# Kernel optimization log

Hardware: AMD Instinct MI355X
Metric: run time of the kernel (lower is better)

## Reference

```python
import jax, jax.numpy as jnp
import numpy as np

B, T, H, L, AS = 64, 256, 1024, 3, 128  # batch, seq-1, hidden, layers, alphabet


def setup_inputs() -> dict:
    key = jax.random.key(0)
    ks = jax.random.split(key, 8)
    # one-hot character sequence (B, T, AS), float32
    idx = jax.random.randint(ks[0], (B, T), 0, AS)
    sequence = jax.nn.one_hot(idx, AS, dtype=jnp.float32)
    u = lambda k, shape, fan: jax.random.uniform(
        k, shape, minval=-1.0 / np.sqrt(fan), maxval=1.0 / np.sqrt(fan), dtype=jnp.float32)
    W_i2h = u(ks[1], (H, AS), AS)
    b_i2h = u(ks[2], (H,), AS)
    # per-layer LSTM params, PyTorch gate order [i, f, g, o]; layer inputs all have width H
    W_ih = u(ks[3], (L, 4 * H, H), H)
    W_hh = u(ks[4], (L, 4 * H, H), H)
    b_ih = u(ks[5], (L, 4 * H), H)
    b_hh = u(ks[6], (L, 4 * H), H)
    W_h2O = u(ks[7], (AS, H), H)
    b_h2O = jnp.zeros((AS,), dtype=jnp.float32)
    h0 = jnp.zeros((L, B, H), dtype=jnp.float32)
    c0 = jnp.zeros((L, B, H), dtype=jnp.float32)
    return dict(sequence=sequence, W_i2h=W_i2h, b_i2h=b_i2h, W_ih=W_ih, W_hh=W_hh,
                b_ih=b_ih, b_hh=b_hh, W_h2O=W_h2O, b_h2O=b_h2O, h0=h0, c0=c0)


def _lstm_layer(x, h0, c0, W_ih, W_hh, b_ih, b_hh):
    # x: (B, T, H). Precompute input contribution to the gates for all steps.
    xg = jnp.einsum('bth,gh->btg', x, W_ih) + b_ih  # (B, T, 4H)

    def step(carry, xg_t):
        h, c = carry
        gates = xg_t + h @ W_hh.T + b_hh  # (B, 4H)
        i, f, g, o = jnp.split(gates, 4, axis=-1)
        c = jax.nn.sigmoid(f) * c + jax.nn.sigmoid(i) * jnp.tanh(g)
        h = jax.nn.sigmoid(o) * jnp.tanh(c)
        return (h, c), h

    (hT, cT), hs = jax.lax.scan(step, (h0, c0), jnp.swapaxes(xg, 0, 1))
    return jnp.swapaxes(hs, 0, 1), hT, cT  # (B,T,H), (B,H), (B,H)


def reference(sequence, W_i2h, b_i2h, W_ih, W_hh, b_ih, b_hh, W_h2O, b_h2O, h0, c0):
    # i2h projection
    x = jnp.einsum('bta,ha->bth', sequence, W_i2h) + b_i2h  # (B, T, H)
    # multi-layer LSTM over x (eval mode: the dropout=True arg is inactive in eval)
    inp = x
    h_fin, c_fin = [], []
    for l in range(L):
        inp, hT, cT = _lstm_layer(inp, h0[l], c0[l], W_ih[l], W_hh[l], b_ih[l], b_hh[l])
        h_fin.append(hT)
        c_fin.append(cT)
    # NOTE: faithful to the original code's bug -- h2O is applied to the i2h
    # output `x`, not to the LSTM output. The LSTM only produces the new hidden.
    out = x.reshape(-1, H) @ W_h2O.T + b_h2O  # (B*T, AS)
    return out, jnp.stack(h_fin), jnp.stack(c_fin)
```

## Files before the change

kernel.cpp:

```cpp
#include <hip/hip_runtime.h>
#include <stdint.h>
#include <stddef.h>

#define B_  64
#define T_  256
#define H_  1024
#define AS_ 128
#define L_  3

typedef __attribute__((ext_vector_type(8))) short bf16x8;
typedef __attribute__((ext_vector_type(4))) float f32x4;
typedef __attribute__((ext_vector_type(4))) unsigned u32x4;

__device__ __forceinline__ unsigned short f2bf(float f) {
  union { float f; unsigned u; } x; x.f = f;
  unsigned r = x.u + 0x7fffu + ((x.u >> 16) & 1u);
  return (unsigned short)(r >> 16);
}
__device__ __forceinline__ float bf2f(unsigned short s) {
  union { unsigned u; float f; } x; x.u = ((unsigned)s) << 16; return x.f;
}
__device__ __forceinline__ float sigmf(float x) { return 1.0f / (1.0f + __expf(-x)); }
__device__ __forceinline__ float tanh_f(float x) {
  x = fminf(fmaxf(x, -15.0f), 15.0f);
  float e = __expf(2.0f * x);
  return (e - 1.0f) / (e + 1.0f);
}

__device__ __forceinline__ void st_u16_cc(unsigned short* p, unsigned short v) {
  __hip_atomic_store(p, v, __ATOMIC_RELAXED, __HIP_MEMORY_SCOPE_AGENT);
}
__device__ __forceinline__ void st_u32_cc(unsigned* p, unsigned v) {
  __hip_atomic_store(p, v, __ATOMIC_RELAXED, __HIP_MEMORY_SCOPE_AGENT);
}
__device__ __forceinline__ unsigned ld_u32_cc(const unsigned* p) {
  return __hip_atomic_load(p, __ATOMIC_RELAXED, __HIP_MEMORY_SCOPE_AGENT);
}
__device__ __forceinline__ u32x4 ld_b128_cc_nw(const void* p) {
  u32x4 r;
  asm volatile("global_load_dwordx4 %0, %1, off sc0 sc1" : "=v"(r) : "v"(p));
  return r;
}
__device__ __forceinline__ void st_b128_cc_nw(void* p, u32x4 v) {
  asm volatile("global_store_dwordx4 %0, %1, off sc0 sc1" :: "v"(p), "v"(v) : "memory");
}
__device__ __forceinline__ void wait_vm4_tie4(u32x4& a, u32x4& b, u32x4& c, u32x4& d) {
  asm volatile("s_waitcnt vmcnt(4)"
               : "+v"(a), "+v"(b), "+v"(c), "+v"(d) :: "memory");
  __builtin_amdgcn_sched_barrier(0);
}
__device__ __forceinline__ void wait_vm0_tie4(u32x4& a, u32x4& b, u32x4& c, u32x4& d) {
  asm volatile("s_waitcnt vmcnt(0)"
               : "+v"(a), "+v"(b), "+v"(c), "+v"(d) :: "memory");
  __builtin_amdgcn_sched_barrier(0);
}
__device__ __forceinline__ void lds_barrier() {
  __builtin_amdgcn_sched_barrier(0);
  asm volatile("s_waitcnt lgkmcnt(0)" ::: "memory");
  __builtin_amdgcn_sched_barrier(0);
  __builtin_amdgcn_s_barrier();
  __builtin_amdgcn_sched_barrier(0);
}


__global__ void k_prep(unsigned* __restrict__ zp, int nzero,
                       const float* __restrict__ Wi2h, const float* __restrict__ bi2h,
                       unsigned short* __restrict__ Wt,
                       const float* __restrict__ Wih, unsigned short* __restrict__ Wihb, int nwih,
                       const float* __restrict__ Wh2o, unsigned short* __restrict__ Wh2ob,
                       const float* __restrict__ bih, const float* __restrict__ bhh,
                       float* __restrict__ bsum) {
  int i = blockIdx.x * 256 + threadIdx.x;
  if (i < nzero) { st_u32_cc(zp + i, 0u); return; }
  i -= nzero;
  if (i < AS_ * H_) { int a = i >> 10, h = i & 1023; Wt[i] = f2bf(Wi2h[h * AS_ + a] + bi2h[h]); return; }
  i -= AS_ * H_;
  if (i < nwih) { Wihb[i] = f2bf(Wih[i]); return; }
  i -= nwih;
  if (i < AS_ * H_) { Wh2ob[i] = f2bf(Wh2o[i]); return; }
  i -= AS_ * H_;
  if (i < L_ * 4 * H_) bsum[i] = bih[i] + bhh[i];
}

__global__ __launch_bounds__(128) void k_gather(const float* __restrict__ seq,
                                                const unsigned short* __restrict__ Wt,
                                                unsigned short* __restrict__ xbf) {
  __shared__ int sidx;
  const int bt = blockIdx.x, tid = threadIdx.x;
  if (seq[(size_t)bt * AS_ + tid] > 0.5f) sidx = tid;
  __syncthreads();
  const int b = bt >> 8, t = bt & 255;
  const uint4* s = (const uint4*)(Wt + (size_t)sidx * H_);
  uint4* d = (uint4*)(xbf + ((size_t)t * B_ + b) * H_);
  d[tid] = s[tid];
}


__device__ __forceinline__ void gld16(const void* g, void* l) {
  __builtin_amdgcn_global_load_lds((const __attribute__((address_space(1))) unsigned int*)g,
                                   (__attribute__((address_space(3))) unsigned int*)l,
                                   16, 0, 0);
}

template <int OUT>
__device__ __forceinline__ void gemm_tile(const unsigned short* __restrict__ A,
                                          const unsigned short* __restrict__ Bm,
                                          const float* __restrict__ bias,
                                          void* __restrict__ Cout,
                                          int m0, int n0, int K, int N, int tid,
                                          unsigned short* As, unsigned short* Bs) {
  const int lane = tid & 63, wv = tid >> 6;
  const int wr = wv >> 1, wc = wv & 1;
  const int kg = lane >> 4, li = lane & 15;
  f32x4 acc[4][4] = {};

  for (int k0 = 0; k0 < K; k0 += 32) {
    for (int i = 0; i < 2; ++i) {
      int c0 = i * 256 + wv * 64;
      int cid = c0 + lane;
      int row = cid >> 2, lc = cid & 3;
      int sc = lc ^ ((row >> 1) & 3);
      gld16(A + (size_t)(m0 + row) * K + k0 + sc * 8, (char*)As + (size_t)c0 * 16);
      gld16(Bm + (size_t)(n0 + row) * K + k0 + sc * 8, (char*)Bs + (size_t)c0 * 16);
    }
    __syncthreads();
    bf16x8 af[4], bfm[4];
#pragma unroll
    for (int mi = 0; mi < 4; ++mi) {
      int row = wr * 64 + mi * 16 + li;
      int pc = kg ^ ((row >> 1) & 3);
      af[mi] = *(const bf16x8*)((const char*)As + row * 64 + pc * 16);
    }
#pragma unroll
    for (int ni = 0; ni < 4; ++ni) {
      int row = wc * 64 + ni * 16 + li;
      int pc = kg ^ ((row >> 1) & 3);
      bfm[ni] = *(const bf16x8*)((const char*)Bs + row * 64 + pc * 16);
    }
#pragma unroll
    for (int mi = 0; mi < 4; ++mi)
#pragma unroll
      for (int ni = 0; ni < 4; ++ni)
        acc[mi][ni] = __builtin_amdgcn_mfma_f32_16x16x32_bf16(af[mi], bfm[ni], acc[mi][ni], 0, 0, 0);
    __syncthreads();
  }

#pragma unroll
  for (int mi = 0; mi < 4; ++mi)
#pragma unroll
    for (int ni = 0; ni < 4; ++ni)
#pragma unroll
      for (int r = 0; r < 4; ++r) {
        int row = m0 + wr * 64 + mi * 16 + kg * 4 + r;
        int col = n0 + wc * 64 + ni * 16 + li;
        float v = acc[mi][ni][r] + bias[col];
        int tt = row >> 6, b = row & 63;
        if (OUT == 4) {
          ((float*)Cout)[(size_t)(b * 256 + tt) * N + col] = v;
        } else {
          int g = col >> 10, u = col & 1023;
          int idx = ((tt * 4 + (b >> 4)) << 16) | ((u >> 5) << 11) |
                    ((b & 15) << 7) | ((u & 31) << 2) | g;
          ((unsigned short*)Cout)[idx] = f2bf(v);
        }
      }
}

template <int OUT>
__global__ __launch_bounds__(256) void k_gemm(const unsigned short* __restrict__ A,
                                              const unsigned short* __restrict__ Bm,
                                              const float* __restrict__ bias,
                                              void* __restrict__ Cout,
                                              int M, int N, int K) {
  __shared__ __align__(16) unsigned short As[128 * 32];
  __shared__ __align__(16) unsigned short Bs[128 * 32];
  gemm_tile<OUT>(A, Bm, bias, Cout, blockIdx.x * 128, blockIdx.y * 128,
                 K, N, threadIdx.x, As, Bs);
}


__global__ __launch_bounds__(256, 1) void k_fused(
    const unsigned short* __restrict__ xgs,
    const float* __restrict__ Whh,
    unsigned short* __restrict__ h_pp,
    unsigned short* __restrict__ out_seq,
    float* __restrict__ hT, float* __restrict__ cT,
    const float* __restrict__ h0, const float* __restrict__ c0,
    unsigned* __restrict__ slots,
    const unsigned short* __restrict__ WihbN,
    const float* __restrict__ bsumN,
    unsigned short* __restrict__ xgs_out,
    const unsigned short* __restrict__ outA,
    const unsigned short* __restrict__ WoutB,
    const float* __restrict__ bout,
    float* __restrict__ outC) {
  __shared__ __align__(16) unsigned short Wlds[64 * 1024];
  __shared__ __align__(16) unsigned short Hs[16 * 1024];
  const int tid = threadIdx.x, lane = tid & 63, w = tid >> 6;
  const int wg = blockIdx.x;

  if (wg >= 128) {
    const int Wp = wg - 128;
    unsigned short* As = Wlds;
    unsigned short* Bs = Wlds + 4096;
    if (outA)
      gemm_tile<4>(outA, WoutB, bout, (void*)outC, Wp * 128, 0, H_, AS_, tid, As, Bs);
    if (WihbN) {
      const int pline = (Wp & 31) * 32;
      for (int k = 0; k < 32; ++k) {
        const int gidx = Wp + k * 128;
        const int mt = gidx >> 5, nt = gidx & 31;
        const unsigned tgt = (unsigned)(2 * mt + 3);
        if (w == 0) {
          const unsigned* base = slots + (lane >> 4) * 1024 + pline + (lane & 15);
          unsigned v0, v1;
          do {
            __builtin_amdgcn_s_sleep(4);
            v0 = ld_u32_cc(base);
            v1 = ld_u32_cc(base + 16);
          } while (__any((int)((v0 < tgt) | (v1 < tgt))));
        }
        __syncthreads();
        gemm_tile<2>(out_seq, WihbN, bsumN, (void*)xgs_out,
                     mt * 128, nt * 128, H_, 4 * H_, tid, As, Bs);
      }
    }
    return;
  }

  const int gb = wg >> 5, ug = wg & 31;
  const int li = lane & 15, kq = lane >> 4;
  const int b  = gb * 16 + li;
  const int u0 = ug * 32 + w * 8 + kq;
  const int u1 = u0 + 4;

  st_u16_cc(&h_pp[((size_t)B_ + b) * H_ + u0], f2bf(h0[(size_t)b * H_ + u0]));
  st_u16_cc(&h_pp[((size_t)B_ + b) * H_ + u1], f2bf(h0[(size_t)b * H_ + u1]));

  bf16x8 afr[32];
  {
    const int r0 = w * 32 + li;
    const float* wr = Whh + ((size_t)(r0 & 3) * H_ + ug * 32 + (r0 >> 2)) * H_ + kq * 8;
#pragma unroll
    for (int ks = 0; ks < 32; ++ks) {
      const float4 f0 = *(const float4*)(wr + ks * 32);
      const float4 f1 = *(const float4*)(wr + ks * 32 + 4);
      union { ushort4 a[2]; bf16x8 v; } uu_;
      uu_.a[0] = ushort4{f2bf(f0.x), f2bf(f0.y), f2bf(f0.z), f2bf(f0.w)};
      uu_.a[1] = ushort4{f2bf(f1.x), f2bf(f1.y), f2bf(f1.z), f2bf(f1.w)};
      afr[ks] = uu_.v;
    }
  }
  for (int it = 0; it < 16; ++it) {
    const int r = w * 32 + 16 + it;
    const float* wr = Whh + ((size_t)(r & 3) * H_ + ug * 32 + (r >> 2)) * H_;
#pragma unroll
    for (int j = 0; j < 4; ++j) {
      const float4 f = *(const float4*)(wr + lane * 16 + j * 4);
      ushort4 p = ushort4{f2bf(f.x), f2bf(f.y), f2bf(f.z), f2bf(f.w)};
      const int k = lane * 16 + j * 4;
      *(ushort4*)((char*)Wlds + (size_t)(w * 16 + it) * 2048 + ((2 * k) ^ ((it & 7) << 4))) = p;
    }
  }
  float cs0 = c0[(size_t)b * H_ + u0], cs1 = c0[(size_t)b * H_ + u1];
  __syncthreads();
  if (w == 3 && lane < 32) {
    st_u32_cc(&slots[gb * 1024 + lane * 32 + ug], 1u);
    asm volatile("s_waitcnt vmcnt(0)" ::: "memory");
  }

  const char* hbase = (const char*)Hs + (size_t)li * 2048;
  const char* wlb   = (const char*)Wlds + (size_t)(w * 16 + li) * 2048;
  const int fxor = (li & 7) << 4;
  const int sb = tid >> 4, seg = tid & 15;
  const int sswz = (sb & 7) << 4;
  char* drow = (char*)Hs + (size_t)sb * 2048;
  unsigned short* exch = Hs;
  const unsigned* myline = slots + gb * 1024 + ug * 32;

  for (int t = 0; t < T_; ++t) {
    const size_t xb2 = ((((size_t)t * 4 + gb) << 16) | (ug << 11) | (li << 7) |
                        ((w * 8 + kq) << 2)) * 2;
    const ushort4 xa = *(const ushort4*)((const char*)xgs + xb2);
    const ushort4 xb = *(const ushort4*)((const char*)xgs + xb2 + 32);

    if (w == 0) {
      const unsigned tgt = (unsigned)(t + 1);
      unsigned v;
      do {
        __builtin_amdgcn_s_sleep(1);
        v = ld_u32_cc(&myline[lane & 31]);
      } while (__any((int)(v < tgt)));
    }
    __syncthreads();

    const char* srcrow = (const char*)(h_pp + (size_t)((t & 1) ^ 1) * (B_ * H_) +
                                       (size_t)(gb * 16 + sb) * H_);
    u32x4 A0 = ld_b128_cc_nw(srcrow +   0 * 256 + seg * 16);
    u32x4 A1 = ld_b128_cc_nw(srcrow +   1 * 256 + seg * 16);
    u32x4 A2 = ld_b128_cc_nw(srcrow +   2 * 256 + seg * 16);
    u32x4 A3 = ld_b128_cc_nw(srcrow +   3 * 256 + seg * 16);
    u32x4 B0 = ld_b128_cc_nw(srcrow + 1024 + 0 * 256 + seg * 16);
    u32x4 B1 = ld_b128_cc_nw(srcrow + 1024 + 1 * 256 + seg * 16);
    u32x4 B2 = ld_b128_cc_nw(srcrow + 1024 + 2 * 256 + seg * 16);
    u32x4 B3 = ld_b128_cc_nw(srcrow + 1024 + 3 * 256 + seg * 16);
    wait_vm4_tie4(A0, A1, A2, A3);
    *(u32x4*)(drow + ((0 * 256 + seg * 16) ^ sswz)) = A0;
    *(u32x4*)(drow + ((1 * 256 + seg * 16) ^ sswz)) = A1;
    *(u32x4*)(drow + ((2 * 256 + seg * 16) ^ sswz)) = A2;
    *(u32x4*)(drow + ((3 * 256 + seg * 16) ^ sswz)) = A3;
    lds_barrier();

    f32x4 a0 = {0.f, 0.f, 0.f, 0.f}, a1 = {0.f, 0.f, 0.f, 0.f};
#pragma unroll
    for (int ks = 0; ks < 16; ++ks) {
      const bf16x8 bb = *(const bf16x8*)(hbase + ((ks * 64 + kq * 16) ^ fxor));
      a0 = __builtin_amdgcn_mfma_f32_16x16x32_bf16(afr[ks], bb, a0, 0, 0, 0);
      const bf16x8 aw = *(const bf16x8*)(wlb + ((ks * 64 + kq * 16) ^ fxor));
      a1 = __builtin_amdgcn_mfma_f32_16x16x32_bf16(aw, bb, a1, 0, 0, 0);
    }

    wait_vm0_tie4(B0, B1, B2, B3);
    *(u32x4*)(drow + ((1024 + 0 * 256 + seg * 16) ^ sswz)) = B0;
    *(u32x4*)(drow + ((1024 + 1 * 256 + seg * 16) ^ sswz)) = B1;
    *(u32x4*)(drow + ((1024 + 2 * 256 + seg * 16) ^ sswz)) = B2;
    *(u32x4*)(drow + ((1024 + 3 * 256 + seg * 16) ^ sswz)) = B3;
    lds_barrier();

#pragma unroll
    for (int ks = 16; ks < 32; ++ks) {
      const bf16x8 bb = *(const bf16x8*)(hbase + ((ks * 64 + kq * 16) ^ fxor));
      a0 = __builtin_amdgcn_mfma_f32_16x16x32_bf16(afr[ks], bb, a0, 0, 0, 0);
      const bf16x8 aw = *(const bf16x8*)(wlb + ((ks * 64 + kq * 16) ^ fxor));
      a1 = __builtin_amdgcn_mfma_f32_16x16x32_bf16(aw, bb, a1, 0, 0, 0);
    }

    float h0v, h1v;
    {
      float gi = a0[0] + bf2f(xa.x), gf = a0[1] + bf2f(xa.y);
      float gg = a0[2] + bf2f(xa.z), go = a0[3] + bf2f(xa.w);
      float ci = sigmf(gf) * cs0 + sigmf(gi) * tanh_f(gg);
      cs0 = ci; h0v = sigmf(go) * tanh_f(ci);
    }
    {
      float gi = a1[0] + bf2f(xb.x), gf = a1[1] + bf2f(xb.y);
      float gg = a1[2] + bf2f(xb.z), go = a1[3] + bf2f(xb.w);
      float ci = sigmf(gf) * cs1 + sigmf(gi) * tanh_f(gg);
      cs1 = ci; h1v = sigmf(go) * tanh_f(ci);
    }
    const unsigned short hb0 = f2bf(h0v), hb1 = f2bf(h1v);

    __syncthreads();
    exch[li * 32 + w * 8 + kq]     = hb0;
    exch[li * 32 + w * 8 + kq + 4] = hb1;
    __syncthreads();

    if (t < T_ - 1) {
      const int bl = tid >> 4, j = tid & 15;
      const unsigned pack = (unsigned)exch[bl * 32 + 2 * j] |
                            ((unsigned)exch[bl * 32 + 2 * j + 1] << 16);
      st_u32_cc((unsigned*)&h_pp[((size_t)(t & 1) * B_ + gb * 16 + bl) * H_ + ug * 32 + 2 * j],
                pack);
    } else {
      hT[(size_t)b * H_ + u0] = h0v; hT[(size_t)b * H_ + u1] = h1v;
      cT[(size_t)b * H_ + u0] = cs0; cT[(size_t)b * H_ + u1] = cs1;
    }
    if (out_seq && tid < 64) {
      const int bo = tid >> 2, q = tid & 3;
      st_b128_cc_nw(&out_seq[((size_t)t * B_ + gb * 16 + bo) * H_ + ug * 32 + 8 * q],
                    *(const u32x4*)&exch[bo * 32 + 8 * q]);
    }
    asm volatile("s_waitcnt vmcnt(0)" ::: "memory");
    __syncthreads();
    if (w == 3 && lane < 32) {
      st_u32_cc(&slots[gb * 1024 + lane * 32 + ug], (unsigned)(t + 2));
      asm volatile("s_waitcnt vmcnt(0)" ::: "memory");
    }
  }
}


extern "C" void kernel_launch(void* const* d_in, const int* in_sizes, int n_in,
                              void* d_out, int out_size, void* d_ws, size_t ws_size,
                              hipStream_t stream) {
  const float* seq  = (const float*)d_in[0];
  const float* Wi2h = (const float*)d_in[1];
  const float* bi2h = (const float*)d_in[2];
  const float* Wih  = (const float*)d_in[3];
  const float* Whh  = (const float*)d_in[4];
  const float* bih  = (const float*)d_in[5];
  const float* bhh  = (const float*)d_in[6];
  const float* Wh2o = (const float*)d_in[7];
  const float* bh2o = (const float*)d_in[8];
  const float* h0   = (const float*)d_in[9];
  const float* c0   = (const float*)d_in[10];
  float* outF = (float*)d_out;

  size_t off = 0;
  auto nb = [&](size_t bytes) { size_t r = off; off += (bytes + 255) & ~(size_t)255; return r; };
  unsigned short* xbf   = (unsigned short*)((char*)d_ws + nb((size_t)B_ * T_ * H_ * 2));
  unsigned short* seqA  = (unsigned short*)((char*)d_ws + nb((size_t)B_ * T_ * H_ * 2));
  unsigned short* xgs   = (unsigned short*)((char*)d_ws + nb((size_t)B_ * T_ * 4 * H_ * 2));
  unsigned short* Wihb  = (unsigned short*)((char*)d_ws + nb((size_t)L_ * 4 * H_ * H_ * 2));
  unsigned short* Wh2ob = (unsigned short*)((char*)d_ws + nb((size_t)AS_ * H_ * 2));
  unsigned short* Wt    = (unsigned short*)((char*)d_ws + nb((size_t)AS_ * H_ * 2));
  float*          bsum  = (float*)((char*)d_ws + nb((size_t)L_ * 4 * H_ * 4));
  unsigned short* h_pp  = (unsigned short*)((char*)d_ws + nb((size_t)2 * B_ * H_ * 2));
  unsigned*       slt   = (unsigned*)((char*)d_ws + nb((size_t)L_ * 4096 * 4));
  (void)ws_size; (void)in_sizes; (void)n_in; (void)out_size;

  const int WLAYER = 4 * H_ * H_;
  const int nzero = L_ * 4096;
  const int nprep = nzero + 2 * AS_ * H_ + L_ * WLAYER + L_ * 4 * H_;

  k_prep<<<(nprep + 255) / 256, 256, 0, stream>>>(
      slt, nzero, Wi2h, bi2h, Wt, Wih, Wihb, L_ * WLAYER, Wh2o, Wh2ob, bih, bhh, bsum);
  k_gather<<<B_ * T_, 128, 0, stream>>>(seq, Wt, xbf);

  k_gemm<2><<<dim3(B_ * T_ / 128, 4 * H_ / 128), 256, 0, stream>>>(
      xbf, Wihb, bsum, (void*)xgs, B_ * T_, 4 * H_, H_);

  float* hT_base = outF + (size_t)B_ * T_ * AS_;
  float* cT_base = hT_base + (size_t)L_ * B_ * H_;

  k_fused<<<256, 256, 0, stream>>>(
      xgs, Whh, h_pp, seqA,
      hT_base, cT_base, h0, c0, slt,
      Wihb + (size_t)1 * WLAYER, bsum + (size_t)1 * 4 * H_, xgs,
      xbf, Wh2ob, bh2o, outF);

  k_fused<<<256, 256, 0, stream>>>(
      xgs, Whh + (size_t)1 * WLAYER, h_pp, xbf,
      hT_base + (size_t)B_ * H_, cT_base + (size_t)B_ * H_,
      h0 + (size_t)B_ * H_, c0 + (size_t)B_ * H_, slt + (size_t)4096,
      Wihb + (size_t)2 * WLAYER, bsum + (size_t)2 * 4 * H_, xgs,
      nullptr, nullptr, nullptr, nullptr);

  k_fused<<<128, 256, 0, stream>>>(
      xgs, Whh + (size_t)2 * WLAYER, h_pp, nullptr,
      hT_base + (size_t)2 * B_ * H_, cT_base + (size_t)2 * B_ * H_,
      h0 + (size_t)2 * B_ * H_, c0 + (size_t)2 * B_ * H_, slt + (size_t)2 * 4096,
      nullptr, nullptr, nullptr, nullptr, nullptr, nullptr, nullptr);
}
```

Before: 3.453 ms.

## Precompute per-character gate and output tables, gather instead of large GEMMs

New measurement: 3.311 ms. 1.04x faster.

```diff
diff --git a/kernel.cpp b/kernel.cpp
--- a/kernel.cpp
+++ b/kernel.cpp
@@ -82,19 +82,6 @@
   if (i < L_ * 4 * H_) bsum[i] = bih[i] + bhh[i];
 }
 
-__global__ __launch_bounds__(128) void k_gather(const float* __restrict__ seq,
-                                                const unsigned short* __restrict__ Wt,
-                                                unsigned short* __restrict__ xbf) {
-  __shared__ int sidx;
-  const int bt = blockIdx.x, tid = threadIdx.x;
-  if (seq[(size_t)bt * AS_ + tid] > 0.5f) sidx = tid;
-  __syncthreads();
-  const int b = bt >> 8, t = bt & 255;
-  const uint4* s = (const uint4*)(Wt + (size_t)sidx * H_);
-  uint4* d = (uint4*)(xbf + ((size_t)t * B_ + b) * H_);
-  d[tid] = s[tid];
-}
-
 
 __device__ __forceinline__ void gld16(const void* g, void* l) {
   __builtin_amdgcn_global_load_lds((const __attribute__((address_space(1))) unsigned int*)g,
@@ -154,10 +141,12 @@
         int row = m0 + wr * 64 + mi * 16 + kg * 4 + r;
         int col = n0 + wc * 64 + ni * 16 + li;
         float v = acc[mi][ni][r] + bias[col];
-        int tt = row >> 6, b = row & 63;
-        if (OUT == 4) {
-          ((float*)Cout)[(size_t)(b * 256 + tt) * N + col] = v;
+        if (OUT == 6) {
+          ((float*)Cout)[(size_t)row * N + col] = v;
+        } else if (OUT == 5) {
+          ((unsigned short*)Cout)[(size_t)row * 4096 + ((col & 1023) << 2) + (col >> 10)] = f2bf(v);
         } else {
+          int tt = row >> 6, b = row & 63;
           int g = col >> 10, u = col & 1023;
           int idx = ((tt * 4 + (b >> 4)) << 16) | ((u >> 5) << 11) |
                     ((b & 15) << 7) | ((u & 31) << 2) | g;
@@ -179,6 +168,27 @@
 }
 
 
+__global__ __launch_bounds__(128) void k_gather2(const float* __restrict__ seq,
+                                                 const unsigned short* __restrict__ Tg,
+                                                 const float* __restrict__ To,
+                                                 unsigned short* __restrict__ xgs,
+                                                 float* __restrict__ outF) {
+  __shared__ int sidx;
+  const int bt = blockIdx.x, tid = threadIdx.x;
+  if (seq[(size_t)bt * AS_ + tid] > 0.5f) sidx = tid;
+  __syncthreads();
+  const int b = bt >> 8, t = bt & 255;
+  outF[(size_t)bt * AS_ + tid] = To[sidx * AS_ + tid];
+  const int ug = tid >> 2, q = tid & 3;
+  const char* src = (const char*)Tg + (size_t)sidx * 8192 + ug * 256 + q * 64;
+  char* dst = (char*)xgs + 2 * ((((size_t)t * 4 + (b >> 4)) << 16) | (ug << 11) | ((b & 15) << 7)) + q * 64;
+  ((uint4*)dst)[0] = ((const uint4*)src)[0];
+  ((uint4*)dst)[1] = ((const uint4*)src)[1];
+  ((uint4*)dst)[2] = ((const uint4*)src)[2];
+  ((uint4*)dst)[3] = ((const uint4*)src)[3];
+}
+
+
 __global__ __launch_bounds__(256, 1) void k_fused(
     const unsigned short* __restrict__ xgs,
     const float* __restrict__ Whh,
@@ -189,11 +199,7 @@
     unsigned* __restrict__ slots,
     const unsigned short* __restrict__ WihbN,
     const float* __restrict__ bsumN,
-    unsigned short* __restrict__ xgs_out,
-    const unsigned short* __restrict__ outA,
-    const unsigned short* __restrict__ WoutB,
-    const float* __restrict__ bout,
-    float* __restrict__ outC) {
+    unsigned short* __restrict__ xgs_out) {
   __shared__ __align__(16) unsigned short Wlds[64 * 1024];
   __shared__ __align__(16) unsigned short Hs[16 * 1024];
   const int tid = threadIdx.x, lane = tid & 63, w = tid >> 6;
@@ -203,8 +209,6 @@
     const int Wp = wg - 128;
     unsigned short* As = Wlds;
     unsigned short* Bs = Wlds + 4096;
-    if (outA)
-      gemm_tile<4>(outA, WoutB, bout, (void*)outC, Wp * 128, 0, H_, AS_, tid, As, Bs);
     if (WihbN) {
       const int pline = (Wp & 31) * 32;
       for (int k = 0; k < 32; ++k) {
@@ -398,7 +402,7 @@
 
   size_t off = 0;
   auto nb = [&](size_t bytes) { size_t r = off; off += (bytes + 255) & ~(size_t)255; return r; };
-  unsigned short* xbf   = (unsigned short*)((char*)d_ws + nb((size_t)B_ * T_ * H_ * 2));
+  unsigned short* bufA  = (unsigned short*)((char*)d_ws + nb((size_t)B_ * T_ * H_ * 2));
   unsigned short* seqA  = (unsigned short*)((char*)d_ws + nb((size_t)B_ * T_ * H_ * 2));
   unsigned short* xgs   = (unsigned short*)((char*)d_ws + nb((size_t)B_ * T_ * 4 * H_ * 2));
   unsigned short* Wihb  = (unsigned short*)((char*)d_ws + nb((size_t)L_ * 4 * H_ * H_ * 2));
@@ -407,6 +411,8 @@
   float*          bsum  = (float*)((char*)d_ws + nb((size_t)L_ * 4 * H_ * 4));
   unsigned short* h_pp  = (unsigned short*)((char*)d_ws + nb((size_t)2 * B_ * H_ * 2));
   unsigned*       slt   = (unsigned*)((char*)d_ws + nb((size_t)L_ * 4096 * 4));
+  unsigned short* Tg    = (unsigned short*)((char*)d_ws + nb((size_t)AS_ * 4096 * 2));
+  float*          To    = (float*)((char*)d_ws + nb((size_t)AS_ * AS_ * 4));
   (void)ws_size; (void)in_sizes; (void)n_in; (void)out_size;
 
   const int WLAYER = 4 * H_ * H_;
@@ -415,10 +421,11 @@
 
   k_prep<<<(nprep + 255) / 256, 256, 0, stream>>>(
       slt, nzero, Wi2h, bi2h, Wt, Wih, Wihb, L_ * WLAYER, Wh2o, Wh2ob, bih, bhh, bsum);
-  k_gather<<<B_ * T_, 128, 0, stream>>>(seq, Wt, xbf);
-
-  k_gemm<2><<<dim3(B_ * T_ / 128, 4 * H_ / 128), 256, 0, stream>>>(
-      xbf, Wihb, bsum, (void*)xgs, B_ * T_, 4 * H_, H_);
+
+  k_gemm<5><<<dim3(1, 32), 256, 0, stream>>>(Wt, Wihb, bsum, (void*)Tg, AS_, 4 * H_, H_);
+  k_gemm<6><<<dim3(1, 1), 256, 0, stream>>>(Wt, Wh2ob, bh2o, (void*)To, AS_, AS_, H_);
+
+  k_gather2<<<B_ * T_, 128, 0, stream>>>(seq, Tg, To, xgs, outF);
 
   float* hT_base = outF + (size_t)B_ * T_ * AS_;
   float* cT_base = hT_base + (size_t)L_ * B_ * H_;
@@ -426,19 +433,17 @@
   k_fused<<<256, 256, 0, stream>>>(
       xgs, Whh, h_pp, seqA,
       hT_base, cT_base, h0, c0, slt,
-      Wihb + (size_t)1 * WLAYER, bsum + (size_t)1 * 4 * H_, xgs,
-      xbf, Wh2ob, bh2o, outF);
+      Wihb + (size_t)1 * WLAYER, bsum + (size_t)1 * 4 * H_, xgs);
 
   k_fused<<<256, 256, 0, stream>>>(
-      xgs, Whh + (size_t)1 * WLAYER, h_pp, xbf,
+      xgs, Whh + (size_t)1 * WLAYER, h_pp, bufA,
       hT_base + (size_t)B_ * H_, cT_base + (size_t)B_ * H_,
       h0 + (size_t)B_ * H_, c0 + (size_t)B_ * H_, slt + (size_t)4096,
-      Wihb + (size_t)2 * WLAYER, bsum + (size_t)2 * 4 * H_, xgs,
-      nullptr, nullptr, nullptr, nullptr);
+      Wihb + (size_t)2 * WLAYER, bsum + (size_t)2 * 4 * H_, xgs);
 
   k_fused<<<128, 256, 0, stream>>>(
       xgs, Whh + (size_t)2 * WLAYER, h_pp, nullptr,
       hT_base + (size_t)2 * B_ * H_, cT_base + (size_t)2 * B_ * H_,
       h0 + (size_t)2 * B_ * H_, c0 + (size_t)2 * B_ * H_, slt + (size_t)2 * 4096,
-      nullptr, nullptr, nullptr, nullptr, nullptr, nullptr, nullptr);
-}
+      nullptr, nullptr, nullptr);
+}
```
